# Optimization experiments

Measured on AMD Instinct MI355X. Metric: run time of the kernel, lower is better.

## Reference

```python
import jax, jax.numpy as jnp
import numpy as np

B, S, HID = 2, 2048, 2048
H, G = 32, 8            # query heads, kv heads
D = HID // H            # head_dim = 64
QPG = H // G            # q heads per kv group = 4


def setup_inputs() -> dict:
    key = jax.random.key(0)
    ks = jax.random.split(key, 5)
    sc = 0.02
    return {
        "x": jax.random.normal(ks[0], (B, S, HID), jnp.float32),
        "Wq": jax.random.normal(ks[1], (HID, HID), jnp.float32) * sc,
        "bq": jnp.zeros((HID,), jnp.float32),
        "Wk": jax.random.normal(ks[2], (HID, G * D), jnp.float32) * sc,
        "bk": jnp.zeros((G * D,), jnp.float32),
        "Wv": jax.random.normal(ks[3], (HID, G * D), jnp.float32) * sc,
        "bv": jnp.zeros((G * D,), jnp.float32),
        "Wo": jax.random.normal(ks[4], (HID, HID), jnp.float32) * sc,
        "bo": jnp.zeros((HID,), jnp.float32),
    }


def reference(x, Wq, bq, Wk, bk, Wv, bv, Wo, bo):
    b, s, _ = x.shape
    # projections (weights stored as [in, out])
    q = (x @ Wq + bq).reshape(b, s, G, QPG, D)      # [b,s,g,p,d]
    k = (x @ Wk + bk).reshape(b, s, G, D)           # [b,s,g,d]
    v = (x @ Wv + bv).reshape(b, s, G, D)
    scale = 1.0 / jnp.sqrt(jnp.asarray(D, x.dtype))
    # grouped attention: repeat_interleave of K/V expressed as shared g axis
    scores = jnp.einsum('bsgpd,btgd->bgpst', q, k) * scale  # [b,g,p,s,t]
    w = jax.nn.softmax(scores, axis=-1)
    o = jnp.einsum('bgpst,btgd->bsgpd', w, v)               # [b,s,g,p,d]
    o = o.reshape(b, s, HID)
    return o @ Wo + bo
```

## Files before the change

### kernel.cpp

```cpp
#include <hip/hip_runtime.h>
#include <hip/hip_bf16.h>


typedef __attribute__((ext_vector_type(8))) short shortx8;
typedef __attribute__((ext_vector_type(4))) float floatx4;

#define SEQ 2048
#define QSC 0.1803368801111204f

#if __has_builtin(__builtin_amdgcn_exp2f)
#define EXP2F(x) __builtin_amdgcn_exp2f(x)
#else
#define EXP2F(x) __expf((x) * 0.6931471805599453f)
#endif

__device__ __forceinline__ unsigned short f2bf(float f) {
  union { float f; unsigned u; } a; a.f = f;
  unsigned u = a.u;
  u += 0x7fffu + ((u >> 16) & 1u);
  return (unsigned short)(u >> 16);
}

__device__ __forceinline__ unsigned cvtpkbf(float lo, float hi) {
  unsigned r;
  asm("v_cvt_pk_bf16_f32 %0, %1, %2" : "=v"(r) : "v"(lo), "v"(hi));
  return r;
}

__device__ __forceinline__ void plswap(unsigned &a, unsigned &b) {
  asm("s_nop 1\n\tv_permlane32_swap_b32 %0, %1" : "+v"(a), "+v"(b));
}
__device__ __forceinline__ void pl16swap(unsigned &a, unsigned &b) {
  asm("s_nop 1\n\tv_permlane16_swap_b32 %0, %1" : "+v"(a), "+v"(b));
}

__device__ __forceinline__ void gload16(const unsigned short* g, unsigned short* l) {
  __builtin_amdgcn_global_load_lds((const __attribute__((address_space(1))) void*)g,
                                   (__attribute__((address_space(3))) void*)l, 16, 0, 0);
}

__global__ __launch_bounds__(256) void prep_kernel(const float* __restrict__ x,
                            const float* __restrict__ Wq, const float* __restrict__ Wk,
                            const float* __restrict__ Wv, const float* __restrict__ Wo,
                            const float* __restrict__ bq, const float* __restrict__ bk,
                            const float* __restrict__ bv,
                            unsigned short* __restrict__ WT,
                            unsigned short* __restrict__ WoT,
                            unsigned short* __restrict__ xb,
                            float* __restrict__ bqkv) {
  const int bid = blockIdx.x, tid = threadIdx.x;
  if (bid < 2560) {
    const float* W; unsigned short* D; int N, ox, oy; float sc = 1.f;
    if (bid < 1024)      { W = Wq; D = WT;               N = 2048; ox = bid & 31;          oy = bid >> 5;          sc = QSC; }
    else if (bid < 1280) { W = Wk; D = WT + 2048 * 2048; N = 512;  ox = (bid - 1024) & 7;  oy = (bid - 1024) >> 3; }
    else if (bid < 1536) { W = Wv; D = WT + 2560 * 2048; N = 512;  ox = (bid - 1280) & 7;  oy = (bid - 1280) >> 3; }
    else                 { W = Wo; D = WoT;              N = 2048; ox = (bid - 1536) & 31; oy = (bid - 1536) >> 5; }
    __shared__ float tile[64][65];
    const int tx = tid & 63, ty = tid >> 6;
    const int r0 = oy * 64, c0 = ox * 64;
#pragma unroll
    for (int i = 0; i < 64; i += 4)
      tile[ty + i][tx] = W[(size_t)(r0 + ty + i) * N + c0 + tx];
    __syncthreads();
#pragma unroll
    for (int i = 0; i < 64; i += 4)
      D[(size_t)(c0 + ty + i) * 2048 + r0 + tx] = f2bf(tile[tx][ty + i] * sc);
    return;
  }
  if (bid < 3584) {
    const size_t base = (size_t)(bid - 2560) * 8192;
#pragma unroll
    for (int k = 0; k < 4; k++) {
      size_t i = base + (size_t)k * 2048 + tid * 8;
      float4 v0 = *(const float4*)(x + i);
      float4 v1 = *(const float4*)(x + i + 4);
      ushort4 o0, o1;
      o0.x = f2bf(v0.x); o0.y = f2bf(v0.y); o0.z = f2bf(v0.z); o0.w = f2bf(v0.w);
      o1.x = f2bf(v1.x); o1.y = f2bf(v1.y); o1.z = f2bf(v1.z); o1.w = f2bf(v1.w);
      *(ushort4*)(xb + i) = o0;
      *(ushort4*)(xb + i + 4) = o1;
    }
    return;
  }
  for (int i = tid; i < 3072; i += 256)
    bqkv[i] = i < 2048 ? bq[i] * QSC : (i < 2560 ? bk[i - 2048] : bv[i - 2560]);
}

template <int MODE>
__global__ __launch_bounds__(256) void gemm_bt(const unsigned short* __restrict__ A,
                                               const unsigned short* __restrict__ BT,
                                               const float* __restrict__ bias,
                                               void* __restrict__ Cout,
                                               unsigned short* __restrict__ Kbuf,
                                               unsigned short* __restrict__ Vt,
                                               int M, int N, int K) {
  __shared__ __align__(16) unsigned short As[128 * 64];
  __shared__ __align__(16) unsigned short Bs[128 * 64];
  const int m0 = blockIdx.x * 128, n0 = blockIdx.y * 128;
  const int tid = threadIdx.x;
  const int lane = tid & 63, wave = tid >> 6;
  const int l15 = lane & 15, quad = lane >> 4;
  const int wm = (wave & 1) * 64, wn = (wave >> 1) * 64;

  const int r8 = lane >> 3;
  const int clog = (lane & 7) ^ r8;
  const unsigned short* aSrc = A + (size_t)(m0 + wave * 32 + r8) * K + clog * 8;
  const unsigned short* bSrc = BT + (size_t)(n0 + wave * 32 + r8) * K + clog * 8;
  unsigned short* aDst = &As[wave * 2048];
  unsigned short* bDst = &Bs[wave * 2048];

  const int s = l15 & 7;
  int aoff[4], boff[4];
#pragma unroll
  for (int i = 0; i < 4; i++) aoff[i] = (wm + i * 16 + l15) * 64 + (quad ^ s) * 8;
#pragma unroll
  for (int j = 0; j < 4; j++) boff[j] = (wn + j * 16 + l15) * 64 + (quad ^ s) * 8;

  floatx4 acc[4][4];
#pragma unroll
  for (int i = 0; i < 4; i++)
#pragma unroll
    for (int j = 0; j < 4; j++)
#pragma unroll
      for (int r = 0; r < 4; r++) acc[i][j][r] = 0.f;

  for (int k0 = 0; k0 < K; k0 += 64) {
    __syncthreads();
#pragma unroll
    for (int j = 0; j < 4; j++) {
      gload16(aSrc + (size_t)j * 8 * K + k0, aDst + j * 512);
      gload16(bSrc + (size_t)j * 8 * K + k0, bDst + j * 512);
    }
    __syncthreads();
    {
      shortx8 af[4], bf[4];
#pragma unroll
      for (int i = 0; i < 4; i++) af[i] = *(const shortx8*)&As[aoff[i]];
#pragma unroll
      for (int j = 0; j < 4; j++) bf[j] = *(const shortx8*)&Bs[boff[j]];
#pragma unroll
      for (int i = 0; i < 4; i++)
#pragma unroll
        for (int j = 0; j < 4; j++)
          acc[i][j] = __builtin_amdgcn_mfma_f32_16x16x32_bf16(af[i], bf[j], acc[i][j], 0, 0, 0);
#pragma unroll
      for (int i = 0; i < 4; i++) af[i] = *(const shortx8*)&As[aoff[i] ^ 32];
#pragma unroll
      for (int j = 0; j < 4; j++) bf[j] = *(const shortx8*)&Bs[boff[j] ^ 32];
#pragma unroll
      for (int i = 0; i < 4; i++)
#pragma unroll
        for (int j = 0; j < 4; j++)
          acc[i][j] = __builtin_amdgcn_mfma_f32_16x16x32_bf16(af[i], bf[j], acc[i][j], 0, 0, 0);
    }
  }

#pragma unroll
  for (int i = 0; i < 4; i++) {
#pragma unroll
    for (int j = 0; j < 4; j++) {
      int col = n0 + wn + j * 16 + l15;
      float bv = bias[col];
#pragma unroll
      for (int r = 0; r < 4; r++) {
        int row = m0 + wm + i * 16 + quad * 4 + r;
        float v = acc[i][j][r] + bv;
        if (MODE == 0) {
          ((float*)Cout)[(size_t)row * N + col] = v;
        } else {
          if (col < 2048) {
            ((unsigned short*)Cout)[(size_t)row * 2048 + col] = f2bf(v);
          } else if (col < 2560) {
            Kbuf[(size_t)row * 512 + (col - 2048)] = f2bf(v);
          } else {
            int g = (col - 2560) >> 6, d = (col - 2560) & 63;
            int b = row >> 11, sidx = row & 2047;
            Vt[(size_t)(((g << 1) | b) * 64 + d) * 2048 + sidx] = f2bf(v);
          }
        }
      }
    }
  }
}

__global__ __launch_bounds__(256, 4) void attn_kernel(const unsigned short* __restrict__ Qb,
                                                      const unsigned short* __restrict__ Kb,
                                                      const unsigned short* __restrict__ Vt,
                                                      unsigned short* __restrict__ O) {
  const int qt = blockIdx.x, g = blockIdx.y, b = blockIdx.z;
  const int tid = threadIdx.x;
  const int lane = tid & 63, wave = tid >> 6;
  const int h = g * 4 + wave;
  const int l15 = lane & 15, quad = lane >> 4;

  __shared__ __align__(16) unsigned short Ks[2][64 * 64];
  __shared__ __align__(16) unsigned short Vs[2][64 * 64];

  shortx8 qf[2][2];
  {
    const unsigned short* qp = Qb + (size_t)(b * SEQ + qt * 32 + l15) * 2048 + h * 64 + quad * 8;
#pragma unroll
    for (int a = 0; a < 2; a++) {
      qf[a][0] = *(const shortx8*)(qp + (size_t)a * 16 * 2048);
      qf[a][1] = *(const shortx8*)(qp + (size_t)a * 16 * 2048 + 32);
    }
  }

  const int r8 = lane >> 3;
  const int clog = (lane & 7) ^ r8;
  const unsigned short* kSrc = Kb + ((size_t)b * SEQ + wave * 16 + r8) * 512 + g * 64 + clog * 8;
  const unsigned short* vSrc = Vt + ((size_t)((g * 2 + b) * 64 + wave * 16 + r8)) * 2048 + clog * 8;

  const int s = l15 & 7;
  int foff[4];
#pragma unroll
  for (int i = 0; i < 4; i++) foff[i] = (i * 16 + l15) * 64 + ((quad ^ s) * 8);

  shortx8 ones;
#pragma unroll
  for (int j = 0; j < 8; j++) ones[j] = (short)0x3F80;

  floatx4 oacc[2][4], lacc[2];
#pragma unroll
  for (int a = 0; a < 2; a++) {
#pragma unroll
    for (int r = 0; r < 4; r++) lacc[a][r] = 0.f;
#pragma unroll
    for (int nd = 0; nd < 4; nd++)
#pragma unroll
      for (int r = 0; r < 4; r++) oacc[a][nd][r] = 0.f;
  }

  {
    unsigned short* kD = &Ks[0][wave * 1024];
    unsigned short* vD = &Vs[0][wave * 1024];
    gload16(kSrc, kD);
    gload16(kSrc + (size_t)8 * 512, kD + 512);
    gload16(vSrc, vD);
    gload16(vSrc + (size_t)8 * 2048, vD + 512);
  }
  __syncthreads();

  for (int it = 0; it < SEQ / 64; it++) {
    const int p = it & 1;
    if (it < SEQ / 64 - 1) {
      const size_t t1 = (size_t)(it + 1) * 64;
      unsigned short* kD = &Ks[p ^ 1][wave * 1024];
      unsigned short* vD = &Vs[p ^ 1][wave * 1024];
      gload16(kSrc + t1 * 512, kD);
      gload16(kSrc + (t1 + 8) * 512, kD + 512);
      gload16(vSrc + t1, vD);
      gload16(vSrc + (size_t)8 * 2048 + t1, vD + 512);
    }

    shortx8 kf[4][2];
#pragma unroll
    for (int i = 0; i < 4; i++) {
      kf[i][0] = *(const shortx8*)&Ks[p][foff[i]];
      kf[i][1] = *(const shortx8*)&Ks[p][foff[i] ^ 32];
    }

    shortx8 pfr[2][2];
#pragma unroll
    for (int a = 0; a < 2; a++) {
      floatx4 sc[4];
      __builtin_amdgcn_s_setprio(1);
#pragma unroll
      for (int i = 0; i < 4; i++) {
        floatx4 c = {0.f, 0.f, 0.f, 0.f};
        c = __builtin_amdgcn_mfma_f32_16x16x32_bf16(kf[i][0], qf[a][0], c, 0, 0, 0);
        c = __builtin_amdgcn_mfma_f32_16x16x32_bf16(kf[i][1], qf[a][1], c, 0, 0, 0);
        sc[i] = c;
      }
      __builtin_amdgcn_s_setprio(0);
      unsigned E00 = cvtpkbf(EXP2F(sc[0][0]), EXP2F(sc[0][1]));
      unsigned E01 = cvtpkbf(EXP2F(sc[0][2]), EXP2F(sc[0][3]));
      unsigned E10 = cvtpkbf(EXP2F(sc[1][0]), EXP2F(sc[1][1]));
      unsigned E11 = cvtpkbf(EXP2F(sc[1][2]), EXP2F(sc[1][3]));
      unsigned E20 = cvtpkbf(EXP2F(sc[2][0]), EXP2F(sc[2][1]));
      unsigned E21 = cvtpkbf(EXP2F(sc[2][2]), EXP2F(sc[2][3]));
      unsigned E30 = cvtpkbf(EXP2F(sc[3][0]), EXP2F(sc[3][1]));
      unsigned E31 = cvtpkbf(EXP2F(sc[3][2]), EXP2F(sc[3][3]));
      plswap(E00, E10); plswap(E01, E11);
      plswap(E20, E30); plswap(E21, E31);
      pl16swap(E00, E10); pl16swap(E01, E11);
      pl16swap(E20, E30); pl16swap(E21, E31);
      union { unsigned u[4]; shortx8 v; } P0, P1;
      P0.u[0] = E00; P0.u[1] = E01; P0.u[2] = E10; P0.u[3] = E11;
      P1.u[0] = E20; P1.u[1] = E21; P1.u[2] = E30; P1.u[3] = E31;
      pfr[a][0] = P0.v;
      pfr[a][1] = P1.v;
    }

    shortx8 vf[4][2];
#pragma unroll
    for (int nd = 0; nd < 4; nd++) {
      vf[nd][0] = *(const shortx8*)&Vs[p][foff[nd]];
      vf[nd][1] = *(const shortx8*)&Vs[p][foff[nd] ^ 32];
    }
#pragma unroll
    for (int a = 0; a < 2; a++) {
#pragma unroll
      for (int ks = 0; ks < 2; ks++) {
        shortx8 pf = pfr[a][ks];
        __builtin_amdgcn_s_setprio(1);
#pragma unroll
        for (int nd = 0; nd < 4; nd++)
          oacc[a][nd] = __builtin_amdgcn_mfma_f32_16x16x32_bf16(vf[nd][ks], pf, oacc[a][nd], 0, 0, 0);
        lacc[a] = __builtin_amdgcn_mfma_f32_16x16x32_bf16(ones, pf, lacc[a], 0, 0, 0);
        __builtin_amdgcn_s_setprio(0);
      }
    }
    __syncthreads();
  }

#pragma unroll
  for (int a = 0; a < 2; a++) {
    float inv = 1.f / lacc[a][0];
    unsigned short* oPtr = O + (size_t)(b * SEQ + qt * 32 + a * 16 + l15) * 2048 + h * 64 + quad * 4;
#pragma unroll
    for (int nd = 0; nd < 4; nd++) {
      uint2 w;
      w.x = (unsigned)f2bf(oacc[a][nd][0] * inv) | ((unsigned)f2bf(oacc[a][nd][1] * inv) << 16);
      w.y = (unsigned)f2bf(oacc[a][nd][2] * inv) | ((unsigned)f2bf(oacc[a][nd][3] * inv) << 16);
      *(uint2*)(oPtr + nd * 16) = w;
    }
  }
}

extern "C" void kernel_launch(void* const* d_in, const int* in_sizes, int n_in,
                              void* d_out, int out_size, void* d_ws, size_t ws_size,
                              hipStream_t stream) {
  const float* x  = (const float*)d_in[0];
  const float* Wq = (const float*)d_in[1];
  const float* bq = (const float*)d_in[2];
  const float* Wk = (const float*)d_in[3];
  const float* bk = (const float*)d_in[4];
  const float* Wv = (const float*)d_in[5];
  const float* bv = (const float*)d_in[6];
  const float* Wo = (const float*)d_in[7];
  const float* bo = (const float*)d_in[8];
  float* out = (float*)d_out;

  char* ws = (char*)d_ws;
  unsigned short* WTall = (unsigned short*)ws;
  unsigned short* WoT   = (unsigned short*)(ws + 12582912);
  float*          bqkv  = (float*)(ws + 20971520);
  unsigned short* xb    = (unsigned short*)(ws + 20987904);
  unsigned short* Qbuf  = (unsigned short*)(ws + 37765120);
  unsigned short* Kbuf  = (unsigned short*)(ws + 54542336);
  unsigned short* Vt    = (unsigned short*)(ws + 58736640);
  unsigned short* Og    = xb;

  prep_kernel<<<dim3(3585), dim3(256), 0, stream>>>(
      x, Wq, Wk, Wv, Wo, bq, bk, bv, WTall, WoT, xb, bqkv);

  gemm_bt<2><<<dim3(32, 24), 256, 0, stream>>>(xb, WTall, bqkv, Qbuf, Kbuf, Vt, 4096, 3072, 2048);

  attn_kernel<<<dim3(64, 8, 2), 256, 0, stream>>>(Qbuf, Kbuf, Vt, Og);

  gemm_bt<0><<<dim3(32, 16), 256, 0, stream>>>(Og, WoT, bo, out, nullptr, nullptr, 4096, 2048, 2048);
}
```

Before: 308.3 us.

## Replace 128x128 GEMM with double-buffered 256x256 tile and interleaved prefetch

Both projection GEMMs move from a 128x128 tile with 256 threads and single-buffered LDS to a 256x256 tile with 512 threads and double-buffered LDS. The next K-slice's global-to-LDS loads are issued in chunks between the MFMA phases, with explicit vmcnt waits, barriers and s_setprio raised around the MFMA blocks. The aim is to hide global load latency behind matrix math and to raise data reuse per LDS byte. In exchange the grid shrinks to 192 and 128 blocks, which leaves many CUs idle on a 256-CU part. The 128KB LDS footprint also limits each CU to one block.

```diff
diff --git a/kernel.cpp b/kernel.cpp
--- a/kernel.cpp
+++ b/kernel.cpp
@@ -87,84 +87,134 @@
 }
 
 template <int MODE>
-__global__ __launch_bounds__(256) void gemm_bt(const unsigned short* __restrict__ A,
-                                               const unsigned short* __restrict__ BT,
-                                               const float* __restrict__ bias,
-                                               void* __restrict__ Cout,
-                                               unsigned short* __restrict__ Kbuf,
-                                               unsigned short* __restrict__ Vt,
-                                               int M, int N, int K) {
-  __shared__ __align__(16) unsigned short As[128 * 64];
-  __shared__ __align__(16) unsigned short Bs[128 * 64];
-  const int m0 = blockIdx.x * 128, n0 = blockIdx.y * 128;
-  const int tid = threadIdx.x;
-  const int lane = tid & 63, wave = tid >> 6;
+__global__ __launch_bounds__(512, 1) void gemm256(const unsigned short* __restrict__ A,
+                                                  const unsigned short* __restrict__ BT,
+                                                  const float* __restrict__ bias,
+                                                  void* __restrict__ Cout,
+                                                  unsigned short* __restrict__ Kbuf,
+                                                  unsigned short* __restrict__ Vt,
+                                                  int M, int N, int K) {
+  __shared__ __align__(16) unsigned short As[2][256 * 64];
+  __shared__ __align__(16) unsigned short Bs[2][256 * 64];
+  const int tid = threadIdx.x, lane = tid & 63, wave = tid >> 6;
+  const int wm = wave >> 2, wn = wave & 3;
   const int l15 = lane & 15, quad = lane >> 4;
-  const int wm = (wave & 1) * 64, wn = (wave >> 1) * 64;
+  const int m0 = blockIdx.x * 256, n0 = blockIdx.y * 256;
 
   const int r8 = lane >> 3;
   const int clog = (lane & 7) ^ r8;
-  const unsigned short* aSrc = A + (size_t)(m0 + wave * 32 + r8) * K + clog * 8;
-  const unsigned short* bSrc = BT + (size_t)(n0 + wave * 32 + r8) * K + clog * 8;
-  unsigned short* aDst = &As[wave * 2048];
-  unsigned short* bDst = &Bs[wave * 2048];
+  const unsigned short* aS = A + (size_t)(m0 + wave * 8 + r8) * K + clog * 8;
+  const unsigned short* bS = BT + (size_t)(n0 + wave * 16 + r8) * K + clog * 8;
+
+#define ISS_A(buf, q, kc) gload16(aS + (size_t)(q) * 64 * K + (kc), &As[buf][(q) * 4096 + wave * 512])
+#define ISS_B(buf, h, j, kc) gload16(bS + (size_t)((h) * 128 + (j) * 8) * K + (kc), &Bs[buf][(h) * 8192 + wave * 1024 + (j) * 512])
 
   const int s = l15 & 7;
-  int aoff[4], boff[4];
-#pragma unroll
-  for (int i = 0; i < 4; i++) aoff[i] = (wm + i * 16 + l15) * 64 + (quad ^ s) * 8;
-#pragma unroll
-  for (int j = 0; j < 4; j++) boff[j] = (wn + j * 16 + l15) * 64 + (quad ^ s) * 8;
-
-  floatx4 acc[4][4];
-#pragma unroll
-  for (int i = 0; i < 4; i++)
+  int aoff[8], boff[4];
+#pragma unroll
+  for (int mi = 0; mi < 8; mi++) aoff[mi] = (wm * 128 + mi * 16 + l15) * 64 + (quad ^ s) * 8;
+#pragma unroll
+  for (int nj = 0; nj < 4; nj++) boff[nj] = (wn * 64 + nj * 16 + l15) * 64 + (quad ^ s) * 8;
+
+  floatx4 acc[8][4];
+#pragma unroll
+  for (int i = 0; i < 8; i++)
 #pragma unroll
     for (int j = 0; j < 4; j++)
 #pragma unroll
       for (int r = 0; r < 4; r++) acc[i][j][r] = 0.f;
 
-  for (int k0 = 0; k0 < K; k0 += 64) {
-    __syncthreads();
-#pragma unroll
-    for (int j = 0; j < 4; j++) {
-      gload16(aSrc + (size_t)j * 8 * K + k0, aDst + j * 512);
-      gload16(bSrc + (size_t)j * 8 * K + k0, bDst + j * 512);
-    }
-    __syncthreads();
-    {
-      shortx8 af[4], bf[4];
-#pragma unroll
-      for (int i = 0; i < 4; i++) af[i] = *(const shortx8*)&As[aoff[i]];
-#pragma unroll
-      for (int j = 0; j < 4; j++) bf[j] = *(const shortx8*)&Bs[boff[j]];
-#pragma unroll
-      for (int i = 0; i < 4; i++)
-#pragma unroll
-        for (int j = 0; j < 4; j++)
-          acc[i][j] = __builtin_amdgcn_mfma_f32_16x16x32_bf16(af[i], bf[j], acc[i][j], 0, 0, 0);
-#pragma unroll
-      for (int i = 0; i < 4; i++) af[i] = *(const shortx8*)&As[aoff[i] ^ 32];
-#pragma unroll
-      for (int j = 0; j < 4; j++) bf[j] = *(const shortx8*)&Bs[boff[j] ^ 32];
-#pragma unroll
-      for (int i = 0; i < 4; i++)
-#pragma unroll
-        for (int j = 0; j < 4; j++)
-          acc[i][j] = __builtin_amdgcn_mfma_f32_16x16x32_bf16(af[i], bf[j], acc[i][j], 0, 0, 0);
-    }
-  }
-
-#pragma unroll
-  for (int i = 0; i < 4; i++) {
-#pragma unroll
-    for (int j = 0; j < 4; j++) {
-      int col = n0 + wn + j * 16 + l15;
+  ISS_A(0, 0, 0); ISS_A(0, 1, 0); ISS_A(0, 2, 0); ISS_A(0, 3, 0);
+  ISS_B(0, 0, 0, 0); ISS_B(0, 0, 1, 0); ISS_B(0, 1, 0, 0); ISS_B(0, 1, 1, 0);
+  asm volatile("s_waitcnt vmcnt(0)" ::: "memory");
+  __builtin_amdgcn_s_barrier();
+  asm volatile("" ::: "memory");
+
+  const int NT = K >> 6;
+  for (int t = 0; t < NT; ++t) {
+    const int b = t & 1;
+    const bool pf = (t + 1 < NT);
+    const int kc1 = (t + 1) << 6;
+    shortx8 af[4], bf0[4], bf1[4];
+
+#pragma unroll
+    for (int i = 0; i < 4; i++) af[i] = *(const shortx8*)&As[b][aoff[i]];
+#pragma unroll
+    for (int j = 0; j < 4; j++) bf0[j] = *(const shortx8*)&Bs[b][boff[j]];
+    if (pf) { ISS_B(b ^ 1, 0, 0, kc1); ISS_B(b ^ 1, 0, 1, kc1); }
+    __builtin_amdgcn_s_barrier();
+    asm volatile("" ::: "memory");
+    __builtin_amdgcn_s_setprio(1);
+#pragma unroll
+    for (int i = 0; i < 4; i++)
+#pragma unroll
+      for (int j = 0; j < 4; j++)
+        acc[i][j] = __builtin_amdgcn_mfma_f32_16x16x32_bf16(af[i], bf0[j], acc[i][j], 0, 0, 0);
+    __builtin_amdgcn_s_setprio(0);
+    __builtin_amdgcn_s_barrier();
+    asm volatile("" ::: "memory");
+
+#pragma unroll
+    for (int i = 0; i < 4; i++) af[i] = *(const shortx8*)&As[b][aoff[i] ^ 32];
+#pragma unroll
+    for (int j = 0; j < 4; j++) bf1[j] = *(const shortx8*)&Bs[b][boff[j] ^ 32];
+    if (pf) { ISS_B(b ^ 1, 1, 0, kc1); ISS_B(b ^ 1, 1, 1, kc1); }
+    __builtin_amdgcn_s_barrier();
+    asm volatile("" ::: "memory");
+    __builtin_amdgcn_s_setprio(1);
+#pragma unroll
+    for (int i = 0; i < 4; i++)
+#pragma unroll
+      for (int j = 0; j < 4; j++)
+        acc[i][j] = __builtin_amdgcn_mfma_f32_16x16x32_bf16(af[i], bf1[j], acc[i][j], 0, 0, 0);
+    __builtin_amdgcn_s_setprio(0);
+    if (pf) { asm volatile("s_waitcnt vmcnt(4)" ::: "memory"); }
+    else    { asm volatile("s_waitcnt vmcnt(0)" ::: "memory"); }
+    __builtin_amdgcn_s_barrier();
+    asm volatile("" ::: "memory");
+
+#pragma unroll
+    for (int i = 0; i < 4; i++) af[i] = *(const shortx8*)&As[b][aoff[4 + i]];
+    if (pf) { ISS_A(b ^ 1, 0, kc1); ISS_A(b ^ 1, 2, kc1); }
+    __builtin_amdgcn_s_barrier();
+    asm volatile("" ::: "memory");
+    __builtin_amdgcn_s_setprio(1);
+#pragma unroll
+    for (int i = 0; i < 4; i++)
+#pragma unroll
+      for (int j = 0; j < 4; j++)
+        acc[4 + i][j] = __builtin_amdgcn_mfma_f32_16x16x32_bf16(af[i], bf0[j], acc[4 + i][j], 0, 0, 0);
+    __builtin_amdgcn_s_setprio(0);
+    __builtin_amdgcn_s_barrier();
+    asm volatile("" ::: "memory");
+
+#pragma unroll
+    for (int i = 0; i < 4; i++) af[i] = *(const shortx8*)&As[b][aoff[4 + i] ^ 32];
+    if (pf) { ISS_A(b ^ 1, 1, kc1); ISS_A(b ^ 1, 3, kc1); }
+    __builtin_amdgcn_s_barrier();
+    asm volatile("" ::: "memory");
+    __builtin_amdgcn_s_setprio(1);
+#pragma unroll
+    for (int i = 0; i < 4; i++)
+#pragma unroll
+      for (int j = 0; j < 4; j++)
+        acc[4 + i][j] = __builtin_amdgcn_mfma_f32_16x16x32_bf16(af[i], bf1[j], acc[4 + i][j], 0, 0, 0);
+    __builtin_amdgcn_s_setprio(0);
+    if (pf) { asm volatile("s_waitcnt vmcnt(2)" ::: "memory"); }
+    __builtin_amdgcn_s_barrier();
+    asm volatile("" ::: "memory");
+  }
+
+#pragma unroll
+  for (int mi = 0; mi < 8; mi++) {
+#pragma unroll
+    for (int nj = 0; nj < 4; nj++) {
+      int col = n0 + wn * 64 + nj * 16 + l15;
       float bv = bias[col];
 #pragma unroll
       for (int r = 0; r < 4; r++) {
-        int row = m0 + wm + i * 16 + quad * 4 + r;
-        float v = acc[i][j][r] + bv;
+        int row = m0 + wm * 128 + mi * 16 + quad * 4 + r;
+        float v = acc[mi][nj][r] + bv;
         if (MODE == 0) {
           ((float*)Cout)[(size_t)row * N + col] = v;
         } else {
@@ -174,13 +224,15 @@
             Kbuf[(size_t)row * 512 + (col - 2048)] = f2bf(v);
           } else {
             int g = (col - 2560) >> 6, d = (col - 2560) & 63;
-            int b = row >> 11, sidx = row & 2047;
-            Vt[(size_t)(((g << 1) | b) * 64 + d) * 2048 + sidx] = f2bf(v);
+            int bb = row >> 11, sidx = row & 2047;
+            Vt[(size_t)(((g << 1) | bb) * 64 + d) * 2048 + sidx] = f2bf(v);
           }
         }
       }
     }
   }
+#undef ISS_A
+#undef ISS_B
 }
 
 __global__ __launch_bounds__(256, 4) void attn_kernel(const unsigned short* __restrict__ Qb,
@@ -355,9 +407,9 @@
   prep_kernel<<<dim3(3585), dim3(256), 0, stream>>>(
       x, Wq, Wk, Wv, Wo, bq, bk, bv, WTall, WoT, xb, bqkv);
 
-  gemm_bt<2><<<dim3(32, 24), 256, 0, stream>>>(xb, WTall, bqkv, Qbuf, Kbuf, Vt, 4096, 3072, 2048);
+  gemm256<2><<<dim3(16, 12), 512, 0, stream>>>(xb, WTall, bqkv, Qbuf, Kbuf, Vt, 4096, 3072, 2048);
 
   attn_kernel<<<dim3(64, 8, 2), 256, 0, stream>>>(Qbuf, Kbuf, Vt, Og);
 
-  gemm_bt<0><<<dim3(32, 16), 256, 0, stream>>>(Og, WoT, bo, out, nullptr, nullptr, 4096, 2048, 2048);
-}
+  gemm256<0><<<dim3(16, 8), 512, 0, stream>>>(Og, WoT, bo, out, nullptr, nullptr, 4096, 2048, 2048);
+}
```

New measurement: 346.6 us. 12.4% more time.
